# Kernel optimization log

Hardware: AMD Instinct MI355X
Metric: run time of the kernel (lower is better)

## Reference

```python
import jax, jax.numpy as jnp
import numpy as np

VOCAB, EMBED = 50000, 256
MODULES, HEADS, HID = 2, 4, 64
B, S = 8, 2048
LABELS = 16


def setup_inputs() -> dict:
    key = jax.random.key(0)
    ks = jax.random.split(key, 12)
    seqs = jax.random.randint(ks[0], (B, S), 0, VOCAB)
    emb = jax.random.normal(ks[1], (VOCAB, EMBED), jnp.float32) * 0.02
    Wq = jax.random.normal(ks[2], (MODULES, HEADS, HID, EMBED), jnp.float32) * (1.0 / np.sqrt(EMBED))
    bq = jax.random.normal(ks[3], (MODULES, HEADS, HID), jnp.float32) * 0.01
    Wk = jax.random.normal(ks[4], (MODULES, HEADS, HID, EMBED), jnp.float32) * (1.0 / np.sqrt(EMBED))
    bk = jax.random.normal(ks[5], (MODULES, HEADS, HID), jnp.float32) * 0.01
    Wv = jax.random.normal(ks[6], (MODULES, HEADS, HID, EMBED), jnp.float32) * (1.0 / np.sqrt(EMBED))
    bv = jax.random.normal(ks[7], (MODULES, HEADS, HID), jnp.float32) * 0.01
    Wz = jax.random.normal(ks[8], (MODULES, EMBED, HEADS * HID), jnp.float32) * (1.0 / np.sqrt(HEADS * HID))
    bz = jax.random.normal(ks[9], (MODULES, EMBED), jnp.float32) * 0.01
    Wo = jax.random.normal(ks[10], (LABELS, S * EMBED), jnp.float32) * (1.0 / np.sqrt(S * EMBED))
    bo = jax.random.normal(ks[11], (LABELS,), jnp.float32) * 0.01
    return {"seqs": seqs, "emb": emb, "Wq": Wq, "bq": bq, "Wk": Wk, "bk": bk,
            "Wv": Wv, "bv": bv, "Wz": Wz, "bz": bz, "Wo": Wo, "bo": bo}


def _forward(seqs, emb, Wq, bq, Wk, bk, Wv, bv, Wz, bz, Wo, bo):
    x = emb[seqs]  # [B, S, E]
    scale = jnp.float32(EMBED) ** 0.5
    for m in range(MODULES):
        # per-head projections with relu (dropout=0 / eval mode)
        Q = jax.nn.relu(jnp.einsum('bse,hde->bhsd', x, Wq[m]) + bq[m][None, :, None, :])
        K = jax.nn.relu(jnp.einsum('bse,hde->bhsd', x, Wk[m]) + bk[m][None, :, None, :])
        V = jax.nn.relu(jnp.einsum('bse,hde->bhsd', x, Wv[m]) + bv[m][None, :, None, :])
        QK = jnp.einsum('bhsd,bhtd->bhst', Q, K) / scale  # [B,H,S,S]
        # double softmax: first over the query axis (torch dim=1 of [B,S,S]),
        # then over the key axis (torch dim=2)
        A = jax.nn.softmax(QK, axis=2)
        A = jax.nn.softmax(A, axis=3)
        Z = jnp.einsum('bhst,bhtd->bhsd', A, V)  # [B,H,S,HID]
        Zall = jnp.transpose(Z, (0, 2, 1, 3)).reshape(x.shape[0], S, HEADS * HID)
        ZF = jnp.einsum('bsk,ek->bse', Zall, Wz[m]) + bz[m]
        x = ZF + x  # residual (layer_norm=False)
    Xf = x.reshape(x.shape[0], S * EMBED)
    y = jax.nn.sigmoid(Xf @ Wo.T + bo)
    return y


def reference(seqs, emb, Wq, bq, Wk, bk, Wv, bv, Wz, bz, Wo, bo):
    return _forward(seqs, emb, Wq, bq, Wk, bk, Wv, bv, Wz, bz, Wo, bo)
```

## Files before the change

### kernel.cpp

```cpp
#include <hip/hip_runtime.h>
#include <math.h>

#define Bb 8
#define Ss 2048
#define Ee 256
#define Hh 4
#define Dd 64

typedef unsigned short u16;
typedef unsigned int u32;
typedef __attribute__((ext_vector_type(8))) short bf16x8;
typedef __attribute__((ext_vector_type(4))) float f32x4;

__device__ __forceinline__ u16 f2bf(float f) {
  union { float f; u32 u; } c; c.f = f;
  return (u16)((c.u + 0x7FFFu + ((c.u >> 16) & 1u)) >> 16);
}
__device__ __forceinline__ float bf2f(u16 u) {
  union { u32 u; float f; } c; c.u = ((u32)u) << 16;
  return c.f;
}
__device__ __forceinline__ float bf2fs(short s) { return bf2f((u16)s); }

__global__ __launch_bounds__(256) void k_w2b(const float* __restrict__ src,
                                             u16* __restrict__ dst) {
  int idx = (blockIdx.x * 256 + threadIdx.x) * 4;
  float4 v = *reinterpret_cast<const float4*>(src + idx);
  ushort4 o;
  o.x = f2bf(v.x); o.y = f2bf(v.y); o.z = f2bf(v.z); o.w = f2bf(v.w);
  *reinterpret_cast<ushort4*>(dst + idx) = o;
}

__global__ __launch_bounds__(256) void k_gather(const int* __restrict__ seqs,
                                                const float* __restrict__ emb,
                                                float* __restrict__ x,
                                                u16* __restrict__ xb) {
  int idx = blockIdx.x * 256 + threadIdx.x;
  int row = idx >> 6, c4 = idx & 63;
  int tok = seqs[row];
  float4 v = reinterpret_cast<const float4*>(emb)[(size_t)tok * 64 + c4];
  reinterpret_cast<float4*>(x)[(size_t)row * 64 + c4] = v;
  ushort4 o;
  o.x = f2bf(v.x); o.y = f2bf(v.y); o.z = f2bf(v.z); o.w = f2bf(v.w);
  reinterpret_cast<ushort4*>(xb)[(size_t)row * 64 + c4] = o;
}

__global__ __launch_bounds__(256) void k_qkvm(const u16* __restrict__ xb,
    const u16* __restrict__ Wqb, const u16* __restrict__ Wkb, const u16* __restrict__ Wvb,
    const float* __restrict__ bq, const float* __restrict__ bk, const float* __restrict__ bv,
    u16* __restrict__ Qf, u16* __restrict__ Kf, u16* __restrict__ Vf, int mod) {
  __shared__ short Xs[128][72];
  __shared__ short Ws[128][72];
  int tid = threadIdx.x;
  int bn = blockIdx.x;
  int arr = bn >> 1, coff = (bn & 1) << 7;
  const u16* W = (arr == 0 ? Wqb : arr == 1 ? Wkb : Wvb) + (size_t)mod * 256 * 256;
  const float* bias = (arr == 0 ? bq : arr == 1 ? bk : bv) + mod * 256;
  u16* Out = (arr == 0 ? Qf : arr == 1 ? Kf : Vf);
  float oscale = (arr == 0) ? 0.0625f : 1.0f;
  int s0 = blockIdx.y * 128;
  int lr = tid >> 1, lc = (tid & 1) << 5;
  int w = tid >> 6, lane = tid & 63, ml = lane & 15, q = lane >> 4;
  int sh = (w >> 1) << 6, th = (w & 1) << 6;
  f32x4 acc[4][4] = {};
  for (int k0 = 0; k0 < 256; k0 += 64) {
#pragma unroll
    for (int hh = 0; hh < 4; hh++) {
      *reinterpret_cast<bf16x8*>(&Xs[lr][lc + hh * 8]) =
          *reinterpret_cast<const bf16x8*>(xb + (size_t)(s0 + lr) * Ee + k0 + lc + hh * 8);
      *reinterpret_cast<bf16x8*>(&Ws[lr][lc + hh * 8]) =
          *reinterpret_cast<const bf16x8*>(W + (size_t)(coff + lr) * Ee + k0 + lc + hh * 8);
    }
    __syncthreads();
#pragma unroll
    for (int ks = 0; ks < 2; ks++) {
      bf16x8 af[4], bfr[4];
#pragma unroll
      for (int mt = 0; mt < 4; mt++)
        af[mt] = *reinterpret_cast<const bf16x8*>(&Xs[sh + mt * 16 + ml][ks * 32 + q * 8]);
#pragma unroll
      for (int nt = 0; nt < 4; nt++)
        bfr[nt] = *reinterpret_cast<const bf16x8*>(&Ws[th + nt * 16 + ml][ks * 32 + q * 8]);
#pragma unroll
      for (int mt = 0; mt < 4; mt++)
#pragma unroll
        for (int nt = 0; nt < 4; nt++)
          acc[mt][nt] = __builtin_amdgcn_mfma_f32_16x16x32_bf16(af[mt], bfr[nt], acc[mt][nt], 0, 0, 0);
    }
    __syncthreads();
  }
#pragma unroll
  for (int mt = 0; mt < 4; mt++)
#pragma unroll
    for (int nt = 0; nt < 4; nt++)
#pragma unroll
      for (int r = 0; r < 4; r++) {
        int gm = s0 + sh + mt * 16 + q * 4 + r;
        int cc = coff + th + nt * 16 + ml;
        float v = acc[mt][nt][r] + bias[cc];
        v = (v > 0.f ? v : 0.f) * oscale;
        Out[(size_t)gm * Ee + cc] = f2bf(v);
      }
}

__global__ __launch_bounds__(256) void k_vt(const u16* __restrict__ Vf,
                                            u16* __restrict__ Vt) {
  __shared__ u16 T[64][72];
  int tid = threadIdx.x;
  int t0 = blockIdx.x * 64;
  int z = blockIdx.y;
  int b = z >> 2, h = z & 3;
  int lr = tid >> 2, lc = (tid & 3) << 4;
#pragma unroll
  for (int hh = 0; hh < 2; hh++) {
    bf16x8 v = *reinterpret_cast<const bf16x8*>(
        Vf + (size_t)(b * Ss + t0 + lr) * Ee + h * Dd + lc + hh * 8);
#pragma unroll
    for (int j = 0; j < 8; j++) T[lr][lc + hh * 8 + j] = (u16)v[j];
  }
  __syncthreads();
#pragma unroll
  for (int j = 0; j < 16; j++) {
    Vt[((size_t)z * Dd + lr) * Ss + t0 + lc + j] = T[lc + j][lr];
  }
}

__global__ __launch_bounds__(256) void k_vsum(const u16* __restrict__ Vt,
                                              float* __restrict__ SV) {
  int z = blockIdx.y;
  int d = blockIdx.x * 4 + (threadIdx.x >> 6);
  int lane = threadIdx.x & 63;
  const u16* row = Vt + ((size_t)z * Dd + d) * Ss;
  float s = 0.f;
#pragma unroll
  for (int it = 0; it < 4; it++) {
    bf16x8 v = *reinterpret_cast<const bf16x8*>(row + it * 512 + lane * 8);
#pragma unroll
    for (int j = 0; j < 8; j++) s += bf2fs(v[j]);
  }
#pragma unroll
  for (int off = 32; off; off >>= 1) s += __shfl_xor(s, off);
  if (lane == 0) SV[(size_t)z * Dd + d] = s;
}

__global__ __launch_bounds__(256) void k_csum(const u16* __restrict__ Qf,
    const u16* __restrict__ Kf, float* __restrict__ llic) {
  __shared__ short Qs[2][128 * 72];
  __shared__ float csm[4][64];
  int tid = threadIdx.x;
  int z = blockIdx.y, b = z >> 2, h = z & 3;
  const u16* Qb = Qf + (size_t)b * Ss * Ee + h * Dd;
  const u16* Kb = Kf + (size_t)b * Ss * Ee + h * Dd;
  int t0 = blockIdx.x * 128;
  int lr = tid >> 1, lc = (tid & 1) << 5;
  int w = tid >> 6, lane = tid & 63, ml = lane & 15, q = lane >> 4;
  int sh = (w >> 1) << 6, th = (w & 1) << 6;
  bf16x8 kb[2][4];
#pragma unroll
  for (int ks = 0; ks < 2; ks++)
#pragma unroll
    for (int nt = 0; nt < 4; nt++)
      kb[ks][nt] = *reinterpret_cast<const bf16x8*>(
          Kb + (size_t)(t0 + th + nt * 16 + ml) * Ee + ks * 32 + q * 8);
  float csum[4] = {};
  int p = 0;
  for (int s0 = 0; s0 < Ss; s0 += 128) {
#pragma unroll
    for (int hh = 0; hh < 4; hh++)
      *reinterpret_cast<bf16x8*>(&Qs[p][lr * 72 + lc + hh * 8]) =
          *reinterpret_cast<const bf16x8*>(Qb + (size_t)(s0 + lr) * Ee + lc + hh * 8);
    __syncthreads();
    f32x4 acc[4][4] = {};
#pragma unroll
    for (int ks = 0; ks < 2; ks++) {
      bf16x8 af[4];
#pragma unroll
      for (int mt = 0; mt < 4; mt++)
        af[mt] = *reinterpret_cast<const bf16x8*>(&Qs[p][(sh + mt * 16 + ml) * 72 + ks * 32 + q * 8]);
#pragma unroll
      for (int mt = 0; mt < 4; mt++)
#pragma unroll
        for (int nt = 0; nt < 4; nt++)
          acc[mt][nt] = __builtin_amdgcn_mfma_f32_16x16x32_bf16(af[mt], kb[ks][nt], acc[mt][nt], 0, 0, 0);
    }
#pragma unroll
    for (int nt = 0; nt < 4; nt++)
#pragma unroll
      for (int mt = 0; mt < 4; mt++)
#pragma unroll
        for (int r = 0; r < 4; r++)
          csum[nt] += __expf(acc[mt][nt][r]);
    p ^= 1;
  }
#pragma unroll
  for (int nt = 0; nt < 4; nt++) {
    csum[nt] += __shfl_xor(csum[nt], 16);
    csum[nt] += __shfl_xor(csum[nt], 32);
  }
  if (lane < 16) {
#pragma unroll
    for (int nt = 0; nt < 4; nt++) csm[w][nt * 16 + ml] = csum[nt];
  }
  __syncthreads();
  if (tid < 128) {
    int half = tid >> 6, c = tid & 63;
    float l = csm[half][c] + csm[half + 2][c];
    llic[(size_t)z * Ss + t0 + half * 64 + c] = -__logf(l);
  }
}

__global__ __launch_bounds__(256) void k_att(const u16* __restrict__ Qf,
    const u16* __restrict__ Kf, const u16* __restrict__ Vt,
    const float* __restrict__ llic, const float* __restrict__ SV,
    u16* __restrict__ Zb) {
  __shared__ short Ks[64 * 72];
  __shared__ short Vs[64 * 72];
  __shared__ short A2s[128 * 76];
  __shared__ float rs_s[2][128];
  int tid = threadIdx.x;
  int z = blockIdx.y, b = z >> 2, h = z & 3;
  const u16* Qb = Qf + (size_t)b * Ss * Ee + h * Dd;
  const u16* Kb = Kf + (size_t)b * Ss * Ee + h * Dd;
  const u16* VtZ = Vt + (size_t)z * Dd * Ss;
  const float* lz = llic + (size_t)z * Ss;
  int s0 = blockIdx.x * 128;
  int w = tid >> 6, lane = tid & 63, ml = lane & 15, q = lane >> 4;
  int wsd = (w >> 1) << 6, wt = (w & 1) << 5;
  bf16x8 qa[2][4];
#pragma unroll
  for (int ks = 0; ks < 2; ks++)
#pragma unroll
    for (int mt = 0; mt < 4; mt++)
      qa[ks][mt] = *reinterpret_cast<const bf16x8*>(
          Qb + (size_t)(s0 + wsd + mt * 16 + ml) * Ee + ks * 32 + q * 8);
  f32x4 acc2[2][4] = {};
  f32x4 rsv[4] = {};
  for (int t0 = 0; t0 < Ss; t0 += 64) {
    __syncthreads();
    if (tid < 128) {
      int r2 = tid >> 1, h2 = (tid & 1) << 5;
#pragma unroll
      for (int j = 0; j < 4; j++)
        *reinterpret_cast<bf16x8*>(&Ks[r2 * 72 + h2 + j * 8]) =
            *reinterpret_cast<const bf16x8*>(Kb + (size_t)(t0 + r2) * Ee + h2 + j * 8);
    } else {
      int t2 = tid - 128;
      int r2 = t2 >> 1, h2 = (t2 & 1) << 5;
#pragma unroll
      for (int j = 0; j < 4; j++)
        *reinterpret_cast<bf16x8*>(&Vs[r2 * 72 + h2 + j * 8]) =
            *reinterpret_cast<const bf16x8*>(VtZ + (size_t)r2 * Ss + t0 + h2 + j * 8);
    }
    __syncthreads();
    f32x4 acc[4][2] = {};
#pragma unroll
    for (int ks = 0; ks < 2; ks++) {
      bf16x8 bf[2];
#pragma unroll
      for (int nt = 0; nt < 2; nt++)
        bf[nt] = *reinterpret_cast<const bf16x8*>(&Ks[(wt + nt * 16 + ml) * 72 + ks * 32 + q * 8]);
#pragma unroll
      for (int mt = 0; mt < 4; mt++)
#pragma unroll
        for (int nt = 0; nt < 2; nt++)
          acc[mt][nt] = __builtin_amdgcn_mfma_f32_16x16x32_bf16(qa[ks][mt], bf[nt], acc[mt][nt], 0, 0, 0);
    }
#pragma unroll
    for (int nt = 0; nt < 2; nt++) {
      float lcv = lz[t0 + wt + nt * 16 + ml];
#pragma unroll
      for (int mt = 0; mt < 4; mt++)
#pragma unroll
        for (int r = 0; r < 4; r++) {
          float e1 = __expf(acc[mt][nt][r] + lcv);
          float p = e1 * (1.f + e1 * (0.5f + e1 * (0.166666667f + e1 * 0.0416666667f)));
          rsv[mt][r] += p;
          union { float f; u32 u; } cv; cv.f = p;
          A2s[(wsd + mt * 16 + q * 4 + r) * 76 + wt + nt * 16 + ml] =
              (short)((cv.u + 0x8000u) >> 16);
        }
    }
    __syncthreads();
#pragma unroll
    for (int ks = 0; ks < 2; ks++) {
      bf16x8 af2[2], bv[4];
#pragma unroll
      for (int mt2 = 0; mt2 < 2; mt2++)
        af2[mt2] = *reinterpret_cast<const bf16x8*>(&A2s[(w * 32 + mt2 * 16 + ml) * 76 + ks * 32 + q * 8]);
#pragma unroll
      for (int nt = 0; nt < 4; nt++)
        bv[nt] = *reinterpret_cast<const bf16x8*>(&Vs[(nt * 16 + ml) * 72 + ks * 32 + q * 8]);
#pragma unroll
      for (int mt2 = 0; mt2 < 2; mt2++)
#pragma unroll
        for (int nt = 0; nt < 4; nt++)
          acc2[mt2][nt] = __builtin_amdgcn_mfma_f32_16x16x32_bf16(af2[mt2], bv[nt], acc2[mt2][nt], 0, 0, 0);
    }
  }
#pragma unroll
  for (int mt = 0; mt < 4; mt++)
#pragma unroll
    for (int r = 0; r < 4; r++) {
      float v = rsv[mt][r];
      v += __shfl_xor(v, 1); v += __shfl_xor(v, 2);
      v += __shfl_xor(v, 4); v += __shfl_xor(v, 8);
      if (ml == 0) rs_s[w & 1][wsd + mt * 16 + q * 4 + r] = v;
    }
  __syncthreads();
  const float* SVz = SV + (size_t)z * Dd;
#pragma unroll
  for (int mt2 = 0; mt2 < 2; mt2++)
#pragma unroll
    for (int r = 0; r < 4; r++) {
      int row = w * 32 + mt2 * 16 + q * 4 + r;
      float inv = 1.f / (2048.f + rs_s[0][row] + rs_s[1][row]);
#pragma unroll
      for (int nt = 0; nt < 4; nt++) {
        float o = (SVz[nt * 16 + ml] + acc2[mt2][nt][r]) * inv;
        Zb[(size_t)(b * Ss + s0 + row) * Ee + h * Dd + nt * 16 + ml] = f2bf(o);
      }
    }
}

__global__ __launch_bounds__(256) void k_zfm(const u16* __restrict__ Zb,
    const u16* __restrict__ Wzb, const float* __restrict__ bzp,
    float* __restrict__ x, u16* __restrict__ xb, int mod) {
  __shared__ short Zs[128][72];
  __shared__ short Ws[128][72];
  int tid = threadIdx.x;
  int coff = blockIdx.x << 7;
  const u16* W = Wzb + (size_t)mod * 256 * 256;
  const float* bias = bzp + mod * Ee;
  int s0 = blockIdx.y * 128;
  int lr = tid >> 1, lc = (tid & 1) << 5;
  int w = tid >> 6, lane = tid & 63, ml = lane & 15, q = lane >> 4;
  int sh = (w >> 1) << 6, th = (w & 1) << 6;
  f32x4 acc[4][4] = {};
  for (int k0 = 0; k0 < 256; k0 += 64) {
#pragma unroll
    for (int hh = 0; hh < 4; hh++) {
      *reinterpret_cast<bf16x8*>(&Zs[lr][lc + hh * 8]) =
          *reinterpret_cast<const bf16x8*>(Zb + (size_t)(s0 + lr) * Ee + k0 + lc + hh * 8);
      *reinterpret_cast<bf16x8*>(&Ws[lr][lc + hh * 8]) =
          *reinterpret_cast<const bf16x8*>(W + (size_t)(coff + lr) * Ee + k0 + lc + hh * 8);
    }
    __syncthreads();
#pragma unroll
    for (int ks = 0; ks < 2; ks++) {
      bf16x8 af[4], bfr[4];
#pragma unroll
      for (int mt = 0; mt < 4; mt++)
        af[mt] = *reinterpret_cast<const bf16x8*>(&Zs[sh + mt * 16 + ml][ks * 32 + q * 8]);
#pragma unroll
      for (int nt = 0; nt < 4; nt++)
        bfr[nt] = *reinterpret_cast<const bf16x8*>(&Ws[th + nt * 16 + ml][ks * 32 + q * 8]);
#pragma unroll
      for (int mt = 0; mt < 4; mt++)
#pragma unroll
        for (int nt = 0; nt < 4; nt++)
          acc[mt][nt] = __builtin_amdgcn_mfma_f32_16x16x32_bf16(af[mt], bfr[nt], acc[mt][nt], 0, 0, 0);
    }
    __syncthreads();
  }
#pragma unroll
  for (int mt = 0; mt < 4; mt++)
#pragma unroll
    for (int nt = 0; nt < 4; nt++)
#pragma unroll
      for (int r = 0; r < 4; r++) {
        int gm = s0 + sh + mt * 16 + q * 4 + r;
        int gn = coff + th + nt * 16 + ml;
        float xv = x[(size_t)gm * Ee + gn] + acc[mt][nt][r] + bias[gn];
        x[(size_t)gm * Ee + gn] = xv;
        xb[(size_t)gm * Ee + gn] = f2bf(xv);
      }
}

__global__ __launch_bounds__(256) void k_final1(const float* __restrict__ x,
    const float* __restrict__ Wo, float* __restrict__ part) {
  int c = blockIdx.x, l = blockIdx.y, b = blockIdx.z;
  int tid = threadIdx.x;
  const float4* xr = reinterpret_cast<const float4*>(x + (size_t)b * (Ss * Ee) + c * 8192);
  const float4* wr = reinterpret_cast<const float4*>(Wo + (size_t)l * (Ss * Ee) + c * 8192);
  float sum = 0.f;
  for (int i = tid; i < 2048; i += 256) {
    float4 a = xr[i], w = wr[i];
    sum += a.x * w.x + a.y * w.y + a.z * w.z + a.w * w.w;
  }
  __shared__ float red[256];
  red[tid] = sum;
  __syncthreads();
  for (int o = 128; o; o >>= 1) {
    if (tid < o) red[tid] += red[tid + o];
    __syncthreads();
  }
  if (tid == 0) part[((b * 16 + l) << 6) + c] = red[0];
}

__global__ void k_final2(const float* __restrict__ part, const float* __restrict__ bo,
                         float* __restrict__ out) {
  int idx = threadIdx.x;
  int b = idx >> 4, l = idx & 15;
  float s = 0.f;
  for (int c = 0; c < 64; c++) s += part[((b * 16 + l) << 6) + c];
  s += bo[l];
  out[idx] = 1.f / (1.f + __expf(-s));
}

extern "C" void kernel_launch(void* const* d_in, const int* in_sizes, int n_in,
                              void* d_out, int out_size, void* d_ws, size_t ws_size,
                              hipStream_t stream) {
  const int*   seqs = (const int*)d_in[0];
  const float* emb  = (const float*)d_in[1];
  const float* Wq   = (const float*)d_in[2];
  const float* bq   = (const float*)d_in[3];
  const float* Wk   = (const float*)d_in[4];
  const float* bk   = (const float*)d_in[5];
  const float* Wv   = (const float*)d_in[6];
  const float* bv   = (const float*)d_in[7];
  const float* Wz   = (const float*)d_in[8];
  const float* bz   = (const float*)d_in[9];
  const float* Wo   = (const float*)d_in[10];
  const float* bo   = (const float*)d_in[11];
  float* out = (float*)d_out;
  float* ws  = (float*)d_ws;

  float* x    = ws;
  u16*   xb   = (u16*)(ws + 4194304);
  u16*   Qf   = (u16*)(ws + 6291456);
  u16*   Kf   = (u16*)(ws + 8388608);
  u16*   Vf   = (u16*)(ws + 10485760);
  u16*   Vt   = (u16*)(ws + 12582912);
  u16*   Zb   = (u16*)(ws + 14680064);
  float* SV   = ws + 16777216;
  float* part = ws + 16779264;
  u16*   Wqb  = (u16*)(ws + 16787456);
  u16*   Wkb  = (u16*)(ws + 16852992);
  u16*   Wvb  = (u16*)(ws + 16918528);
  u16*   Wzb  = (u16*)(ws + 16984064);
  float* llic = ws + 17049600;

  k_gather<<<(Bb * Ss * 64) / 256, 256, 0, stream>>>(seqs, emb, x, xb);
  k_w2b<<<131072 / 1024, 256, 0, stream>>>(Wq, Wqb);
  k_w2b<<<131072 / 1024, 256, 0, stream>>>(Wk, Wkb);
  k_w2b<<<131072 / 1024, 256, 0, stream>>>(Wv, Wvb);
  k_w2b<<<131072 / 1024, 256, 0, stream>>>(Wz, Wzb);

  for (int m = 0; m < 2; m++) {
    k_qkvm<<<dim3(6, 128), 256, 0, stream>>>(xb, Wqb, Wkb, Wvb, bq, bk, bv, Qf, Kf, Vf, m);
    k_vt<<<dim3(32, 32), 256, 0, stream>>>(Vf, Vt);
    k_vsum<<<dim3(16, 32), 256, 0, stream>>>(Vt, SV);
    k_csum<<<dim3(16, 32), 256, 0, stream>>>(Qf, Kf, llic);
    k_att<<<dim3(16, 32), 256, 0, stream>>>(Qf, Kf, Vt, llic, SV, Zb);
    k_zfm<<<dim3(2, 128), 256, 0, stream>>>(Zb, Wzb, bz, x, xb, m);
  }

  k_final1<<<dim3(64, 16, 8), 256, 0, stream>>>(x, Wo, part);
  k_final2<<<1, 128, 0, stream>>>(part, bo, out);
}
```

Before: 521.3 us.

## Restructure column-sum and attention kernels around 32x32 MFMA with split-S atomics

The column-sum kernel now splits the query range in two, accumulates partial sums into a zeroed buffer with atomics, and takes the log in a separate small kernel. It also uses 32x32x16 MFMAs with Q read directly from global memory instead of staged through LDS. The attention kernel moves to 64-row tiles with 32x32 MFMAs, keeps K in registers with next-tile prefetch, double-buffers V in LDS, and remaps workgroups across XCDs. Exp is replaced by exp2, with log2e folded into the Q scale, and packed bf16 conversion is used. The aims are more parallelism, fewer LDS round trips and cheaper transcendentals, at the cost of an extra launch, atomics, and changed rounding.

```diff
diff --git a/kernel.cpp b/kernel.cpp
--- a/kernel.cpp
+++ b/kernel.cpp
@@ -11,6 +11,7 @@
 typedef unsigned int u32;
 typedef __attribute__((ext_vector_type(8))) short bf16x8;
 typedef __attribute__((ext_vector_type(4))) float f32x4;
+typedef __attribute__((ext_vector_type(16))) float f32x16;
 
 __device__ __forceinline__ u16 f2bf(float f) {
   union { float f; u32 u; } c; c.f = f;
@@ -21,6 +22,12 @@
   return c.f;
 }
 __device__ __forceinline__ float bf2fs(short s) { return bf2f((u16)s); }
+__device__ __forceinline__ u32 cvtpk(float a, float b) {
+  u32 r;
+  asm("v_cvt_pk_bf16_f32 %0, %1, %2" : "=v"(r) : "v"(a), "v"(b));
+  return r;
+}
+__device__ __forceinline__ float ex2(float x) { return __builtin_amdgcn_exp2f(x); }
 
 __global__ __launch_bounds__(256) void k_w2b(const float* __restrict__ src,
                                              u16* __restrict__ dst) {
@@ -57,7 +64,7 @@
   const u16* W = (arr == 0 ? Wqb : arr == 1 ? Wkb : Wvb) + (size_t)mod * 256 * 256;
   const float* bias = (arr == 0 ? bq : arr == 1 ? bk : bv) + mod * 256;
   u16* Out = (arr == 0 ? Qf : arr == 1 ? Kf : Vf);
-  float oscale = (arr == 0) ? 0.0625f : 1.0f;
+  float oscale = (arr == 0) ? 0.0625f * 1.44269504f : 1.0f;
   int s0 = blockIdx.y * 128;
   int lr = tid >> 1, lc = (tid & 1) << 5;
   int w = tid >> 6, lane = tid & 63, ml = lane & 15, q = lane >> 4;
@@ -126,7 +133,10 @@
 }
 
 __global__ __launch_bounds__(256) void k_vsum(const u16* __restrict__ Vt,
-                                              float* __restrict__ SV) {
+                                              float* __restrict__ SV,
+                                              float* __restrict__ csums) {
+  int gi = (blockIdx.y * gridDim.x + blockIdx.x) * 256 + threadIdx.x;
+  if (gi < 32 * Ss) csums[gi] = 0.f;
   int z = blockIdx.y;
   int d = blockIdx.x * 4 + (threadIdx.x >> 6);
   int lane = threadIdx.x & 63;
@@ -143,182 +153,169 @@
   if (lane == 0) SV[(size_t)z * Dd + d] = s;
 }
 
-__global__ __launch_bounds__(256) void k_csum(const u16* __restrict__ Qf,
-    const u16* __restrict__ Kf, float* __restrict__ llic) {
-  __shared__ short Qs[2][128 * 72];
-  __shared__ float csm[4][64];
-  int tid = threadIdx.x;
-  int z = blockIdx.y, b = z >> 2, h = z & 3;
+__global__ __launch_bounds__(256, 4) void k_csum(const u16* __restrict__ Qf,
+    const u16* __restrict__ Kf, float* __restrict__ csums) {
+  __shared__ float csm[2][128];
+  int tid = threadIdx.x;
+  int lin = (blockIdx.z * 2 + blockIdx.y) * 16 + blockIdx.x;
+  int wgid = (lin & 7) * 128 + (lin >> 3);
+  int ttile = wgid & 15, shalf = (wgid >> 4) & 1, z = wgid >> 5;
+  int b = z >> 2, h = z & 3;
   const u16* Qb = Qf + (size_t)b * Ss * Ee + h * Dd;
   const u16* Kb = Kf + (size_t)b * Ss * Ee + h * Dd;
-  int t0 = blockIdx.x * 128;
-  int lr = tid >> 1, lc = (tid & 1) << 5;
-  int w = tid >> 6, lane = tid & 63, ml = lane & 15, q = lane >> 4;
+  int w = tid >> 6, lane = tid & 63, l31 = lane & 31, hi = lane >> 5;
   int sh = (w >> 1) << 6, th = (w & 1) << 6;
+  const u16* kr = Kb + (size_t)(ttile * 128 + th + l31) * Ee + hi * 8;
   bf16x8 kb[2][4];
 #pragma unroll
-  for (int ks = 0; ks < 2; ks++)
-#pragma unroll
-    for (int nt = 0; nt < 4; nt++)
-      kb[ks][nt] = *reinterpret_cast<const bf16x8*>(
-          Kb + (size_t)(t0 + th + nt * 16 + ml) * Ee + ks * 32 + q * 8);
-  float csum[4] = {};
-  int p = 0;
-  for (int s0 = 0; s0 < Ss; s0 += 128) {
-#pragma unroll
-    for (int hh = 0; hh < 4; hh++)
-      *reinterpret_cast<bf16x8*>(&Qs[p][lr * 72 + lc + hh * 8]) =
-          *reinterpret_cast<const bf16x8*>(Qb + (size_t)(s0 + lr) * Ee + lc + hh * 8);
-    __syncthreads();
-    f32x4 acc[4][4] = {};
-#pragma unroll
-    for (int ks = 0; ks < 2; ks++) {
-      bf16x8 af[4];
-#pragma unroll
-      for (int mt = 0; mt < 4; mt++)
-        af[mt] = *reinterpret_cast<const bf16x8*>(&Qs[p][(sh + mt * 16 + ml) * 72 + ks * 32 + q * 8]);
-#pragma unroll
-      for (int mt = 0; mt < 4; mt++)
-#pragma unroll
-        for (int nt = 0; nt < 4; nt++)
-          acc[mt][nt] = __builtin_amdgcn_mfma_f32_16x16x32_bf16(af[mt], kb[ks][nt], acc[mt][nt], 0, 0, 0);
-    }
-#pragma unroll
-    for (int nt = 0; nt < 4; nt++)
-#pragma unroll
-      for (int mt = 0; mt < 4; mt++)
-#pragma unroll
-        for (int r = 0; r < 4; r++)
-          csum[nt] += __expf(acc[mt][nt][r]);
-    p ^= 1;
-  }
-#pragma unroll
-  for (int nt = 0; nt < 4; nt++) {
-    csum[nt] += __shfl_xor(csum[nt], 16);
-    csum[nt] += __shfl_xor(csum[nt], 32);
-  }
-  if (lane < 16) {
-#pragma unroll
-    for (int nt = 0; nt < 4; nt++) csm[w][nt * 16 + ml] = csum[nt];
+  for (int tt = 0; tt < 2; tt++)
+#pragma unroll
+    for (int kk = 0; kk < 4; kk++)
+      kb[tt][kk] = *reinterpret_cast<const bf16x8*>(kr + (size_t)tt * 32 * Ee + kk * 16);
+  float cs0 = 0.f, cs1 = 0.f;
+  int sBeg = shalf * 1024, sEnd = sBeg + 1024;
+  for (int s0 = sBeg; s0 < sEnd; s0 += 128) {
+#pragma unroll
+    for (int qs = 0; qs < 2; qs++) {
+      const u16* Qr = Qb + (size_t)(s0 + sh + qs * 32 + l31) * Ee + hi * 8;
+      f32x16 a0 = {}, a1 = {};
+      __builtin_amdgcn_s_setprio(1);
+#pragma unroll
+      for (int kk = 0; kk < 4; kk++) {
+        bf16x8 qv = *reinterpret_cast<const bf16x8*>(Qr + kk * 16);
+        a0 = __builtin_amdgcn_mfma_f32_32x32x16_bf16(qv, kb[0][kk], a0, 0, 0, 0);
+        a1 = __builtin_amdgcn_mfma_f32_32x32x16_bf16(qv, kb[1][kk], a1, 0, 0, 0);
+      }
+      __builtin_amdgcn_s_setprio(0);
+#pragma unroll
+      for (int j = 0; j < 16; j++) { cs0 += ex2(a0[j]); cs1 += ex2(a1[j]); }
+    }
+  }
+  cs0 += __shfl_xor(cs0, 32);
+  cs1 += __shfl_xor(cs1, 32);
+  if (lane < 32) {
+    csm[w >> 1][th + l31] = cs0;
+    csm[w >> 1][th + 32 + l31] = cs1;
   }
   __syncthreads();
-  if (tid < 128) {
-    int half = tid >> 6, c = tid & 63;
-    float l = csm[half][c] + csm[half + 2][c];
-    llic[(size_t)z * Ss + t0 + half * 64 + c] = -__logf(l);
-  }
-}
-
-__global__ __launch_bounds__(256) void k_att(const u16* __restrict__ Qf,
+  if (tid < 128)
+    atomicAdd(&csums[(size_t)z * Ss + ttile * 128 + tid], csm[0][tid] + csm[1][tid]);
+}
+
+__global__ void k_llog(float* __restrict__ llic) {
+  int i = blockIdx.x * 256 + threadIdx.x;
+  llic[i] = -__log2f(llic[i]);
+}
+
+__global__ __launch_bounds__(256, 4) void k_att(const u16* __restrict__ Qf,
     const u16* __restrict__ Kf, const u16* __restrict__ Vt,
     const float* __restrict__ llic, const float* __restrict__ SV,
     u16* __restrict__ Zb) {
-  __shared__ short Ks[64 * 72];
-  __shared__ short Vs[64 * 72];
-  __shared__ short A2s[128 * 76];
-  __shared__ float rs_s[2][128];
-  int tid = threadIdx.x;
-  int z = blockIdx.y, b = z >> 2, h = z & 3;
+  __shared__ short Vs[2][64 * 72];
+  __shared__ short A2s[64 * 72];
+  __shared__ float rs_s[2][64];
+  int tid = threadIdx.x;
+  int lin = blockIdx.y * 32 + blockIdx.x;
+  int wgid = (lin & 7) * 128 + (lin >> 3);
+  int z = wgid >> 5, sblk = wgid & 31;
+  int b = z >> 2, h = z & 3;
   const u16* Qb = Qf + (size_t)b * Ss * Ee + h * Dd;
   const u16* Kb = Kf + (size_t)b * Ss * Ee + h * Dd;
   const u16* VtZ = Vt + (size_t)z * Dd * Ss;
   const float* lz = llic + (size_t)z * Ss;
-  int s0 = blockIdx.x * 128;
-  int w = tid >> 6, lane = tid & 63, ml = lane & 15, q = lane >> 4;
-  int wsd = (w >> 1) << 6, wt = (w & 1) << 5;
-  bf16x8 qa[2][4];
-#pragma unroll
-  for (int ks = 0; ks < 2; ks++)
-#pragma unroll
-    for (int mt = 0; mt < 4; mt++)
-      qa[ks][mt] = *reinterpret_cast<const bf16x8*>(
-          Qb + (size_t)(s0 + wsd + mt * 16 + ml) * Ee + ks * 32 + q * 8);
-  f32x4 acc2[2][4] = {};
-  f32x4 rsv[4] = {};
+  int s0 = sblk * 64;
+  int w = tid >> 6, lane = tid & 63;
+  int l31 = lane & 31, hi = lane >> 5;
+  int tw = w >> 1, sw = w & 1;
+  const u16* qrow = Qb + (size_t)(s0 + sw * 32 + l31) * Ee + hi * 8;
+  bf16x8 qb0 = *reinterpret_cast<const bf16x8*>(qrow);
+  bf16x8 qb1 = *reinterpret_cast<const bf16x8*>(qrow + 16);
+  bf16x8 qb2 = *reinterpret_cast<const bf16x8*>(qrow + 32);
+  bf16x8 qb3 = *reinterpret_cast<const bf16x8*>(qrow + 48);
+  const u16* krow = Kb + (size_t)(tw * 32 + l31) * Ee + hi * 8;
+  bf16x8 kf0 = *reinterpret_cast<const bf16x8*>(krow);
+  bf16x8 kf1 = *reinterpret_cast<const bf16x8*>(krow + 16);
+  bf16x8 kf2 = *reinterpret_cast<const bf16x8*>(krow + 32);
+  bf16x8 kf3 = *reinterpret_cast<const bf16x8*>(krow + 48);
+  int sd = tid >> 2, sg = (tid & 3) << 4;
+  {
+    const u16* vsrc = VtZ + (size_t)sd * Ss + sg;
+    *reinterpret_cast<bf16x8*>(&Vs[0][sd * 72 + sg]) = *reinterpret_cast<const bf16x8*>(vsrc);
+    *reinterpret_cast<bf16x8*>(&Vs[0][sd * 72 + sg + 8]) = *reinterpret_cast<const bf16x8*>(vsrc + 8);
+  }
+  f32x16 acc2 = {};
+  float rsv = 0.f;
+  int pb = 0;
+  short* arow = &A2s[(sw * 32 + l31) * 72 + tw * 32];
+  const short* a2row = &A2s[(tw * 32 + l31) * 72 + hi * 8];
   for (int t0 = 0; t0 < Ss; t0 += 64) {
-    __syncthreads();
-    if (tid < 128) {
-      int r2 = tid >> 1, h2 = (tid & 1) << 5;
-#pragma unroll
-      for (int j = 0; j < 4; j++)
-        *reinterpret_cast<bf16x8*>(&Ks[r2 * 72 + h2 + j * 8]) =
-            *reinterpret_cast<const bf16x8*>(Kb + (size_t)(t0 + r2) * Ee + h2 + j * 8);
-    } else {
-      int t2 = tid - 128;
-      int r2 = t2 >> 1, h2 = (t2 & 1) << 5;
-#pragma unroll
-      for (int j = 0; j < 4; j++)
-        *reinterpret_cast<bf16x8*>(&Vs[r2 * 72 + h2 + j * 8]) =
-            *reinterpret_cast<const bf16x8*>(VtZ + (size_t)r2 * Ss + t0 + h2 + j * 8);
-    }
-    __syncthreads();
-    f32x4 acc[4][2] = {};
-#pragma unroll
-    for (int ks = 0; ks < 2; ks++) {
-      bf16x8 bf[2];
-#pragma unroll
-      for (int nt = 0; nt < 2; nt++)
-        bf[nt] = *reinterpret_cast<const bf16x8*>(&Ks[(wt + nt * 16 + ml) * 72 + ks * 32 + q * 8]);
-#pragma unroll
-      for (int mt = 0; mt < 4; mt++)
-#pragma unroll
-        for (int nt = 0; nt < 2; nt++)
-          acc[mt][nt] = __builtin_amdgcn_mfma_f32_16x16x32_bf16(qa[ks][mt], bf[nt], acc[mt][nt], 0, 0, 0);
-    }
-#pragma unroll
-    for (int nt = 0; nt < 2; nt++) {
-      float lcv = lz[t0 + wt + nt * 16 + ml];
-#pragma unroll
-      for (int mt = 0; mt < 4; mt++)
-#pragma unroll
-        for (int r = 0; r < 4; r++) {
-          float e1 = __expf(acc[mt][nt][r] + lcv);
-          float p = e1 * (1.f + e1 * (0.5f + e1 * (0.166666667f + e1 * 0.0416666667f)));
-          rsv[mt][r] += p;
-          union { float f; u32 u; } cv; cv.f = p;
-          A2s[(wsd + mt * 16 + q * 4 + r) * 76 + wt + nt * 16 + ml] =
-              (short)((cv.u + 0x8000u) >> 16);
-        }
-    }
-    __syncthreads();
-#pragma unroll
-    for (int ks = 0; ks < 2; ks++) {
-      bf16x8 af2[2], bv[4];
-#pragma unroll
-      for (int mt2 = 0; mt2 < 2; mt2++)
-        af2[mt2] = *reinterpret_cast<const bf16x8*>(&A2s[(w * 32 + mt2 * 16 + ml) * 76 + ks * 32 + q * 8]);
-#pragma unroll
-      for (int nt = 0; nt < 4; nt++)
-        bv[nt] = *reinterpret_cast<const bf16x8*>(&Vs[(nt * 16 + ml) * 72 + ks * 32 + q * 8]);
-#pragma unroll
-      for (int mt2 = 0; mt2 < 2; mt2++)
-#pragma unroll
-        for (int nt = 0; nt < 4; nt++)
-          acc2[mt2][nt] = __builtin_amdgcn_mfma_f32_16x16x32_bf16(af2[mt2], bv[nt], acc2[mt2][nt], 0, 0, 0);
-    }
-  }
-#pragma unroll
-  for (int mt = 0; mt < 4; mt++)
-#pragma unroll
-    for (int r = 0; r < 4; r++) {
-      float v = rsv[mt][r];
-      v += __shfl_xor(v, 1); v += __shfl_xor(v, 2);
-      v += __shfl_xor(v, 4); v += __shfl_xor(v, 8);
-      if (ml == 0) rs_s[w & 1][wsd + mt * 16 + q * 4 + r] = v;
-    }
+    f32x16 at = {};
+    __builtin_amdgcn_s_setprio(1);
+    at = __builtin_amdgcn_mfma_f32_32x32x16_bf16(kf0, qb0, at, 0, 0, 0);
+    at = __builtin_amdgcn_mfma_f32_32x32x16_bf16(kf1, qb1, at, 0, 0, 0);
+    at = __builtin_amdgcn_mfma_f32_32x32x16_bf16(kf2, qb2, at, 0, 0, 0);
+    at = __builtin_amdgcn_mfma_f32_32x32x16_bf16(kf3, qb3, at, 0, 0, 0);
+    __builtin_amdgcn_s_setprio(0);
+    int tn = (t0 + 64 < Ss) ? t0 + 64 : 0;
+    {
+      const u16* krn = krow + (size_t)tn * Ee;
+      kf0 = *reinterpret_cast<const bf16x8*>(krn);
+      kf1 = *reinterpret_cast<const bf16x8*>(krn + 16);
+      kf2 = *reinterpret_cast<const bf16x8*>(krn + 32);
+      kf3 = *reinterpret_cast<const bf16x8*>(krn + 48);
+    }
+#pragma unroll
+    for (int g = 0; g < 4; g++) {
+      const float4 lc = *reinterpret_cast<const float4*>(lz + t0 + tw * 32 + g * 8 + hi * 4);
+      float e0 = ex2(at[g * 4 + 0] + lc.x);
+      float e1 = ex2(at[g * 4 + 1] + lc.y);
+      float e2 = ex2(at[g * 4 + 2] + lc.z);
+      float e3 = ex2(at[g * 4 + 3] + lc.w);
+      float p0 = e0 * (1.f + e0 * (0.5f + e0 * (0.166666667f + e0 * 0.0416666667f)));
+      float p1 = e1 * (1.f + e1 * (0.5f + e1 * (0.166666667f + e1 * 0.0416666667f)));
+      float p2 = e2 * (1.f + e2 * (0.5f + e2 * (0.166666667f + e2 * 0.0416666667f)));
+      float p3 = e3 * (1.f + e3 * (0.5f + e3 * (0.166666667f + e3 * 0.0416666667f)));
+      rsv += (p0 + p1) + (p2 + p3);
+      uint2 pk;
+      pk.x = cvtpk(p0, p1);
+      pk.y = cvtpk(p2, p3);
+      *reinterpret_cast<uint2*>(arow + g * 8 + hi * 4) = pk;
+    }
+    __syncthreads();
+    {
+      const u16* vsrc = VtZ + (size_t)sd * Ss + tn + sg;
+      bf16x8 v0 = *reinterpret_cast<const bf16x8*>(vsrc);
+      bf16x8 v1 = *reinterpret_cast<const bf16x8*>(vsrc + 8);
+      short* vdst = &Vs[pb ^ 1][sd * 72 + sg];
+      *reinterpret_cast<bf16x8*>(vdst) = v0;
+      *reinterpret_cast<bf16x8*>(vdst + 8) = v1;
+    }
+    {
+      const short* vrow = &Vs[pb][(sw * 32 + l31) * 72 + hi * 8];
+      __builtin_amdgcn_s_setprio(1);
+#pragma unroll
+      for (int kk = 0; kk < 4; kk++) {
+        bf16x8 af2 = *reinterpret_cast<const bf16x8*>(a2row + kk * 16);
+        bf16x8 bvv = *reinterpret_cast<const bf16x8*>(vrow + kk * 16);
+        acc2 = __builtin_amdgcn_mfma_f32_32x32x16_bf16(af2, bvv, acc2, 0, 0, 0);
+      }
+      __builtin_amdgcn_s_setprio(0);
+    }
+    __syncthreads();
+    pb ^= 1;
+  }
+  rsv += __shfl_xor(rsv, 32);
+  if (lane < 32) rs_s[tw][sw * 32 + l31] = rsv;
   __syncthreads();
-  const float* SVz = SV + (size_t)z * Dd;
-#pragma unroll
-  for (int mt2 = 0; mt2 < 2; mt2++)
-#pragma unroll
-    for (int r = 0; r < 4; r++) {
-      int row = w * 32 + mt2 * 16 + q * 4 + r;
+  float svd = SV[(size_t)z * Dd + sw * 32 + l31];
+#pragma unroll
+  for (int g = 0; g < 4; g++)
+#pragma unroll
+    for (int rr = 0; rr < 4; rr++) {
+      int row = tw * 32 + g * 8 + hi * 4 + rr;
       float inv = 1.f / (2048.f + rs_s[0][row] + rs_s[1][row]);
-#pragma unroll
-      for (int nt = 0; nt < 4; nt++) {
-        float o = (SVz[nt * 16 + ml] + acc2[mt2][nt][r]) * inv;
-        Zb[(size_t)(b * Ss + s0 + row) * Ee + h * Dd + nt * 16 + ml] = f2bf(o);
-      }
+      float o = (svd + acc2[g * 4 + rr]) * inv;
+      Zb[(size_t)(b * Ss + s0 + row) * Ee + h * Dd + sw * 32 + l31] = f2bf(o);
     }
 }
 
@@ -449,9 +446,10 @@
   for (int m = 0; m < 2; m++) {
     k_qkvm<<<dim3(6, 128), 256, 0, stream>>>(xb, Wqb, Wkb, Wvb, bq, bk, bv, Qf, Kf, Vf, m);
     k_vt<<<dim3(32, 32), 256, 0, stream>>>(Vf, Vt);
-    k_vsum<<<dim3(16, 32), 256, 0, stream>>>(Vt, SV);
-    k_csum<<<dim3(16, 32), 256, 0, stream>>>(Qf, Kf, llic);
-    k_att<<<dim3(16, 32), 256, 0, stream>>>(Qf, Kf, Vt, llic, SV, Zb);
+    k_vsum<<<dim3(16, 32), 256, 0, stream>>>(Vt, SV, llic);
+    k_csum<<<dim3(16, 2, 32), 256, 0, stream>>>(Qf, Kf, llic);
+    k_llog<<<256, 256, 0, stream>>>(llic);
+    k_att<<<dim3(32, 32), 256, 0, stream>>>(Qf, Kf, Vt, llic, SV, Zb);
     k_zfm<<<dim3(2, 128), 256, 0, stream>>>(Zb, Wzb, bz, x, xb, m);
   }
 
```

Result: no change. 526.4 us (+1.0%).
